# Kernel tuning notes

Measured on AMD Instinct MI355X. Metric: run time of the kernel, lower is better.

The kernel has to match this reference:

```python
import jax, jax.numpy as jnp
import numpy as np

D_MODEL = 1024
N_HEADS = 16
HEAD_DIM = D_MODEL // N_HEADS
ROPE_THETA = 10000.0


def setup_inputs() -> dict:
    key = jax.random.key(0)
    ks = jax.random.split(key, 5)
    B, S = 4, 2048
    x = jax.random.normal(ks[0], (B, S, D_MODEL), dtype=jnp.float32)
    Wq = jax.random.normal(ks[1], (D_MODEL, D_MODEL), dtype=jnp.float32) * 0.02
    Wk = jax.random.normal(ks[2], (D_MODEL, D_MODEL), dtype=jnp.float32) * 0.02
    Wv = jax.random.normal(ks[3], (D_MODEL, D_MODEL), dtype=jnp.float32) * 0.02
    Wo = jax.random.normal(ks[4], (D_MODEL, D_MODEL), dtype=jnp.float32) * 0.02
    token_positions = jnp.arange(S, dtype=jnp.int32)
    return {"x": x, "token_positions": token_positions, "Wq": Wq, "Wk": Wk, "Wv": Wv, "Wo": Wo}


def apply_rope(t, positions):
    # t: [B, H, S, Dk]; positions: [S]
    half = HEAD_DIM // 2
    inv_freq = 1.0 / (ROPE_THETA ** (jnp.arange(half, dtype=jnp.float32) * 2.0 / HEAD_DIM))
    angles = positions.astype(jnp.float32)[:, None] * inv_freq[None, :]  # [S, half]
    cos = jnp.cos(angles)[None, None]  # [1,1,S,half]
    sin = jnp.sin(angles)[None, None]
    t_even = t[..., 0::2]
    t_odd = t[..., 1::2]
    rot_even = t_even * cos - t_odd * sin
    rot_odd = t_even * sin + t_odd * cos
    out = jnp.stack([rot_even, rot_odd], axis=-1)  # [B,H,S,half,2]
    return out.reshape(t.shape)


def reference(x, token_positions, Wq, Wk, Wv, Wo):
    B, S, _ = x.shape
    H, Dk = N_HEADS, HEAD_DIM
    # QKV projections, split heads -> [B, H, S, Dk]
    q = (x @ Wq).reshape(B, S, H, Dk).transpose(0, 2, 1, 3)
    k = (x @ Wk).reshape(B, S, H, Dk).transpose(0, 2, 1, 3)
    v = (x @ Wv).reshape(B, S, H, Dk).transpose(0, 2, 1, 3)
    q = apply_rope(q, token_positions)
    k = apply_rope(k, token_positions)
    scale = 1.0 / jnp.sqrt(jnp.asarray(Dk, dtype=x.dtype))
    scores = jnp.einsum('bhqd,bhkd->bhqk', q, k) * scale
    causal = jnp.tril(jnp.ones((S, S), dtype=bool))
    scores = jnp.where(causal[None, None], scores, jnp.asarray(-jnp.inf, dtype=scores.dtype))
    attn = jax.nn.softmax(scores, axis=-1)
    ctx = jnp.einsum('bhqk,bhkd->bhqd', attn, v)  # [B,H,S,Dk]
    ctx = ctx.transpose(0, 2, 1, 3).reshape(B, S, H * Dk)
    return ctx @ Wo
```

## Files before the change

kernel.cpp:

```cpp
#include <hip/hip_runtime.h>

typedef unsigned short u16;
typedef unsigned int   u32;
typedef __bf16  bf16x8 __attribute__((ext_vector_type(8)));
typedef float   f32x4  __attribute__((ext_vector_type(4)));
typedef float   f32x16 __attribute__((ext_vector_type(16)));
typedef u16     u16x4  __attribute__((ext_vector_type(4)));
typedef u16     u16x8  __attribute__((ext_vector_type(8)));
typedef u32     u32x4  __attribute__((ext_vector_type(4)));

#define D_MODEL 1024
#define N_HEADS 16
#define HEAD_DIM 64
#define BATCH 4
#define SEQ 2048
#define MROWS (BATCH*SEQ)

__device__ __forceinline__ u16 f2bf(float f){
  unsigned u = __builtin_bit_cast(unsigned, f);
  u += 0x7fffu + ((u >> 16) & 1u);
  return (u16)(u >> 16);
}
__device__ __forceinline__ float bf2f(u16 h){
  unsigned u = ((unsigned)h) << 16;
  return __builtin_bit_cast(float, u);
}
__device__ __forceinline__ u32 cvtpk(float a, float b){
  u32 r; asm("v_cvt_pk_bf16_f32 %0, %1, %2" : "=v"(r) : "v"(a), "v"(b)); return r;
}
__device__ __forceinline__ void gload_lds16(const u16* g, u16* l){
  __builtin_amdgcn_global_load_lds((const __attribute__((address_space(1))) void*)g,
                                   (__attribute__((address_space(3))) void*)l, 16, 0, 0);
}

__global__ void k_cvt_x(const float* __restrict__ x, u16* __restrict__ xb, int n4){
  int i = blockIdx.x * 256 + threadIdx.x;
  if (i >= n4) return;
  float4 v = reinterpret_cast<const float4*>(x)[i];
  u16x4 o;
  o.x = f2bf(v.x); o.y = f2bf(v.y); o.z = f2bf(v.z); o.w = f2bf(v.w);
  *reinterpret_cast<u16x4*>(xb + (size_t)i * 4) = o;
}

__global__ void k_transpose_w(const float* __restrict__ Wq, const float* __restrict__ Wk,
                              const float* __restrict__ Wv, const float* __restrict__ Wo,
                              u16* __restrict__ wt){
  __shared__ float t[32][33];
  int z = blockIdx.z;
  const float* W = (z==0)?Wq:(z==1)?Wk:(z==2)?Wv:Wo;
  u16* O = wt + (size_t)z * (D_MODEL*(size_t)D_MODEL);
  int n0 = blockIdx.x*32, k0 = blockIdx.y*32;
  int tx = threadIdx.x, ty = threadIdx.y;
  #pragma unroll
  for (int i = ty; i < 32; i += 8) t[i][tx] = W[(size_t)(k0+i)*D_MODEL + n0 + tx];
  __syncthreads();
  #pragma unroll
  for (int i = ty; i < 32; i += 8){
    int n = n0 + i;
    int np = n;
    if (z < 2){ int d = n & 63; np = (n & ~63) | ((d & 1) << 5) | (d >> 1); }
    O[(size_t)np*D_MODEL + k0 + tx] = f2bf(t[tx][i]);
  }
}

__global__ void k_rope_tab(const int* __restrict__ pos, float2* __restrict__ tab){
  int i = blockIdx.x * 256 + threadIdx.x;
  int s = i >> 5, f = i & 31;
  float inv = exp2f(-(float)f * (13.287712379549449f / 32.0f));
  float a = (float)pos[s] * inv;
  float sn, cs;
  sincosf(a, &sn, &cs);
  tab[i] = make_float2(cs, sn);
}

template<int MODE>
__global__ __launch_bounds__(256, 4) void k_gemm3(const u16* __restrict__ A, const u16* __restrict__ Bt,
                                                  const float2* __restrict__ tab,
                                                  u16* __restrict__ qout, u16* __restrict__ kout,
                                                  u16* __restrict__ vout, float* __restrict__ fout){
  __shared__ u16 sh[3*8192];
  const int K = 1024;
  int tid = threadIdx.x, lane = tid & 63, w = tid >> 6;
  int lr = lane & 15, lg = lane >> 4;
  int m0 = blockIdx.x * 128, n0 = blockIdx.y * 128;
  int wm = w >> 1, wn = w & 1;
  int srow = lane >> 2, scol = (lane & 3) * 8;
  const u16* ga = A  + (size_t)(m0 + w*16 + srow)*K + scol;
  const u16* gb = Bt + (size_t)(n0 + w*16 + srow)*K + scol;
  f32x4 acc[4][4] = {};

#define STG(off, t) { u16* Sb = sh + (off); \
    gload_lds16(ga + (size_t)(t)*32,        Sb + w*512); \
    gload_lds16(ga + (size_t)(t)*32 + 64*K, Sb + 2048 + w*512); \
    gload_lds16(gb + (size_t)(t)*32,        Sb + 4096 + w*512); \
    gload_lds16(gb + (size_t)(t)*32 + 64*K, Sb + 6144 + w*512); }

#define CMP(off) { const u16* Sb = sh + (off); \
    bf16x8 af[4], bv[4]; \
    _Pragma("unroll") \
    for (int mi = 0; mi < 4; mi++) \
      af[mi] = *(const bf16x8*)&Sb[(wm*64 + mi*16 + lr)*32 + lg*8]; \
    _Pragma("unroll") \
    for (int ni = 0; ni < 4; ni++) \
      bv[ni] = *(const bf16x8*)&Sb[4096 + (wn*64 + ni*16 + lr)*32 + lg*8]; \
    _Pragma("unroll") \
    for (int mi = 0; mi < 4; mi++){ \
      _Pragma("unroll") \
      for (int ni = 0; ni < 4; ni++) \
        acc[mi][ni] = __builtin_amdgcn_mfma_f32_16x16x32_bf16(af[mi], bv[ni], acc[mi][ni], 0, 0, 0); \
    } }

  STG(0, 0)
  STG(8192, 1)
  int oc = 0, on = 8192, os = 16384;
  #pragma unroll 1
  for (int t = 0; t < 31; ++t){
    asm volatile("s_waitcnt vmcnt(4) lgkmcnt(0)" ::: "memory");
    __builtin_amdgcn_s_barrier();
    __builtin_amdgcn_sched_barrier(0);
    if (t < 30){ STG(os, t+2) }
    CMP(oc)
    int tmp = oc; oc = on; on = os; os = tmp;
  }
  asm volatile("s_waitcnt vmcnt(0) lgkmcnt(0)" ::: "memory");
  __builtin_amdgcn_s_barrier();
  __builtin_amdgcn_sched_barrier(0);
  CMP(oc)
#undef STG
#undef CMP

  const int which = n0 >> 10;
  #pragma unroll
  for (int mi = 0; mi < 4; mi++){
    int row = m0 + wm*64 + mi*16 + lg*4;
    #pragma unroll
    for (int ni = 0; ni < 4; ni++){
      int col = n0 + wn*64 + ni*16 + lr;
      f32x4 vv = acc[mi][ni];
      if (MODE == 1){
        #pragma unroll
        for (int r = 0; r < 4; r++)
          fout[(size_t)(row + r)*1024 + col] = vv[r];
      } else {
        int cm = col & 1023;
        int hh = cm >> 6, d = cm & 63;
        f32x4 vp = acc[mi][ni ^ 2];
        #pragma unroll
        for (int r = 0; r < 4; r++){
          int rr = row + r;
          int bb = rr >> 11, s = rr & (SEQ-1);
          float val = vv[r];
          if (which < 2){
            float e = (ni < 2) ? val : vp[r];
            float o = (ni < 2) ? vp[r] : val;
            float2 cs = tab[s*32 + ((ni & 1) << 4) + lr];
            float ov = (ni < 2) ? (e*cs.x - o*cs.y) : (e*cs.y + o*cs.x);
            if (which == 0){
              ov *= 0.18033688011112042f;
              qout[(size_t)rr*1024 + cm] = f2bf(ov);
            } else {
              kout[(((size_t)(bb*N_HEADS + hh))*SEQ + s)*64 + d] = f2bf(ov);
            }
          } else {
            vout[(((size_t)(bb*N_HEADS + hh))*(SEQ/16) + (s >> 4))*1024 + d*16 + (s & 15)] = f2bf(val);
          }
        }
      }
    }
  }
}

__global__ __launch_bounds__(256, 3) void k_attn(const u16* __restrict__ q, const u16* __restrict__ k2,
                                                 const u16* __restrict__ v2, u16* __restrict__ ctx){
  __shared__ u16 kv[2][4096];
  const int lane = threadIdx.x & 63, w = threadIdx.x >> 6;
  const int lq = lane & 31, hl = lane >> 5;
  const int B = blockIdx.x;
  const int bh = B & 63, g = 15 - (B >> 6);
  const int b = bh >> 4, h = bh & 15;
  const int qi = 4*g + w;
  const int q0 = qi * 32;
  const int qmax0 = (4*g + 3) * 32;
  const u16* kglob = k2 + (size_t)bh*SEQ*64;
  const u16* vglob = v2 + (size_t)bh*(SEQ/16)*1024;

  const u16* qr_ = q + (size_t)(b*SEQ + q0 + lq)*D_MODEL + h*HEAD_DIM + hl*8;
  bf16x8 qf0 = *(const bf16x8*)&qr_[0];
  bf16x8 qf1 = *(const bf16x8*)&qr_[16];
  bf16x8 qf2 = *(const bf16x8*)&qr_[32];
  bf16x8 qf3 = *(const bf16x8*)&qr_[48];
  f32x16 acc0 = {}, acc1 = {};
  float m = -3.0e38f, l = 0.f;

  auto STAGE = [&](int bf, int jt){
    const u16* ks = kglob + (size_t)(jt + (w<<3) + (lane>>3))*64 + (((lane&7)^(lane>>3))<<3);
    gload_lds16(ks, &kv[bf][w<<9]);
    const u16* vs = vglob + ((size_t)(jt>>4)<<10) + (w<<9) + (lane<<3);
    gload_lds16(vs, &kv[bf][2048 + (w<<9)]);
  };

  STAGE(0, 0);
  __syncthreads();
  int p = 0;
  for (int j0 = 0; j0 <= qmax0; j0 += 32){
    if (j0 + 32 <= qmax0) STAGE(p^1, j0 + 32);
    if (j0 <= q0){
      const char* kb = (const char*)&kv[p][0];
      bf16x8 kf0 = *(const bf16x8*)(kb + lq*128 + (((0+hl) ^ (lq&7))<<4));
      bf16x8 kf1 = *(const bf16x8*)(kb + lq*128 + (((2+hl) ^ (lq&7))<<4));
      bf16x8 kf2 = *(const bf16x8*)(kb + lq*128 + (((4+hl) ^ (lq&7))<<4));
      bf16x8 kf3 = *(const bf16x8*)(kb + lq*128 + (((6+hl) ^ (lq&7))<<4));
      const char* vb = kb + 4096;
      bf16x8 vf00 = *(const bf16x8*)(vb + lq*32 + hl*16);
      bf16x8 vf01 = *(const bf16x8*)(vb + lq*32 + hl*16 + 1024);
      bf16x8 vf10 = *(const bf16x8*)(vb + lq*32 + hl*16 + 2048);
      bf16x8 vf11 = *(const bf16x8*)(vb + lq*32 + hl*16 + 3072);

      f32x16 S = {};
      S = __builtin_amdgcn_mfma_f32_32x32x16_bf16(kf0, qf0, S, 0, 0, 0);
      S = __builtin_amdgcn_mfma_f32_32x32x16_bf16(kf1, qf1, S, 0, 0, 0);
      S = __builtin_amdgcn_mfma_f32_32x32x16_bf16(kf2, qf2, S, 0, 0, 0);
      S = __builtin_amdgcn_mfma_f32_32x32x16_bf16(kf3, qf3, S, 0, 0, 0);

      if (j0 == q0){
        #pragma unroll
        for (int r = 0; r < 16; ++r){
          int kk = (r & 3) + 8*(r >> 2) + 4*hl;
          if (kk > lq) S[r] = -3.0e38f;
        }
      }
      float a0 = fmaxf(fmaxf(S[0],S[1]),  fmaxf(S[2],S[3]));
      float a1 = fmaxf(fmaxf(S[4],S[5]),  fmaxf(S[6],S[7]));
      float a2 = fmaxf(fmaxf(S[8],S[9]),  fmaxf(S[10],S[11]));
      float a3 = fmaxf(fmaxf(S[12],S[13]),fmaxf(S[14],S[15]));
      float pm = fmaxf(fmaxf(a0,a1), fmaxf(a2,a3));
      pm = fmaxf(pm, __shfl_xor(pm, 32));
      if (__any(pm > m + 8.f)){
        float mn = fmaxf(m, pm);
        float cr = __builtin_amdgcn_exp2f(m - mn);
        l *= cr;
        #pragma unroll
        for (int r = 0; r < 16; ++r){ acc0[r] *= cr; acc1[r] *= cr; }
        m = mn;
      }
      #pragma unroll
      for (int r = 0; r < 16; ++r) S[r] = __builtin_amdgcn_exp2f(S[r] - m);
      float s0_ = (S[0]+S[1]) + (S[2]+S[3]);
      float s1_ = (S[4]+S[5]) + (S[6]+S[7]);
      float s2_ = (S[8]+S[9]) + (S[10]+S[11]);
      float s3_ = (S[12]+S[13]) + (S[14]+S[15]);
      l += (s0_+s1_) + (s2_+s3_);
      u32 g0a = cvtpk(S[0], S[1]),  g0b = cvtpk(S[2], S[3]);
      u32 g1a = cvtpk(S[4], S[5]),  g1b = cvtpk(S[6], S[7]);
      u32 g2a = cvtpk(S[8], S[9]),  g2b = cvtpk(S[10],S[11]);
      u32 g3a = cvtpk(S[12],S[13]), g3b = cvtpk(S[14],S[15]);
      u32 s0a = hl ? g0a : g1a, s0b = hl ? g0b : g1b;
      u32 e0a = (u32)__shfl_xor((int)s0a, 32), e0b = (u32)__shfl_xor((int)s0b, 32);
      u32 m0a = hl ? g1a : g0a, m0b = hl ? g1b : g0b;
      u32 s1a = hl ? g2a : g3a, s1b = hl ? g2b : g3b;
      u32 e1a = (u32)__shfl_xor((int)s1a, 32), e1b = (u32)__shfl_xor((int)s1b, 32);
      u32 m1a = hl ? g3a : g2a, m1b = hl ? g3b : g2b;
      u32x4 A0 = { hl ? e0a : m0a, hl ? e0b : m0b, hl ? m0a : e0a, hl ? m0b : e0b };
      u32x4 A1 = { hl ? e1a : m1a, hl ? e1b : m1b, hl ? m1a : e1a, hl ? m1b : e1b };
      bf16x8 pa0 = __builtin_bit_cast(bf16x8, A0);
      bf16x8 pa1 = __builtin_bit_cast(bf16x8, A1);
      acc0 = __builtin_amdgcn_mfma_f32_32x32x16_bf16(vf00, pa0, acc0, 0, 0, 0);
      acc0 = __builtin_amdgcn_mfma_f32_32x32x16_bf16(vf10, pa1, acc0, 0, 0, 0);
      acc1 = __builtin_amdgcn_mfma_f32_32x32x16_bf16(vf01, pa0, acc1, 0, 0, 0);
      acc1 = __builtin_amdgcn_mfma_f32_32x32x16_bf16(vf11, pa1, acc1, 0, 0, 0);
    }
    __syncthreads();
    p ^= 1;
  }
  l += __shfl_xor(l, 32);
  float inv = __builtin_amdgcn_rcpf(l);
  char* tbc = (char*)kv + w*4096;
  #pragma unroll
  for (int r = 0; r < 16; ++r){
    int d0 = (r & 3) + 8*(r >> 2) + 4*hl;
    *(u16*)(tbc + lq*128 + ((2*d0)      ^ ((lq & 7) << 4))) = f2bf(acc0[r] * inv);
    *(u16*)(tbc + lq*128 + ((2*(d0+32)) ^ ((lq & 7) << 4))) = f2bf(acc1[r] * inv);
  }
  int qr2 = lane >> 1, chb = (lane & 1) * 4;
  u16* cp = ctx + (size_t)(b*SEQ + q0 + qr2)*D_MODEL + h*HEAD_DIM;
  #pragma unroll
  for (int i = 0; i < 4; ++i){
    int ch = chb + i;
    u16x8 vv = *(const u16x8*)(tbc + qr2*128 + 16*(ch ^ (qr2 & 7)));
    *(u16x8*)&cp[ch*8] = vv;
  }
}

extern "C" void kernel_launch(void* const* d_in, const int* in_sizes, int n_in,
                              void* d_out, int out_size, void* d_ws, size_t ws_size,
                              hipStream_t stream){
  const float* x  = (const float*)d_in[0];
  const int*  pos = (const int*)d_in[1];
  const float* Wq = (const float*)d_in[2];
  const float* Wk = (const float*)d_in[3];
  const float* Wv = (const float*)d_in[4];
  const float* Wo = (const float*)d_in[5];
  float* out = (float*)d_out;
  char* ws = (char*)d_ws;
  u16* xb   = (u16*)(ws);
  u16* wt   = (u16*)(ws + 16777216);
  u16* qb   = (u16*)(ws + 25165824);
  u16* kbh  = (u16*)(ws + 41943040);
  u16* vt2  = (u16*)(ws + 58720256);
  float2* tab = (float2*)(ws + 75497472);
  u16* ctxb = xb;

  k_cvt_x<<<(MROWS*D_MODEL/4)/256, 256, 0, stream>>>(x, xb, MROWS*D_MODEL/4);
  k_transpose_w<<<dim3(32,32,4), dim3(32,8), 0, stream>>>(Wq, Wk, Wv, Wo, wt);
  k_rope_tab<<<(SEQ*32)/256, 256, 0, stream>>>(pos, tab);
  k_gemm3<0><<<dim3(64,24), 256, 0, stream>>>(xb, wt, tab, qb, kbh, vt2, nullptr);
  k_attn<<<dim3(1024), 256, 0, stream>>>(qb, kbh, vt2, ctxb);
  k_gemm3<1><<<dim3(64,8), 256, 0, stream>>>(ctxb, wt + 3145728, nullptr, nullptr, nullptr, nullptr, out);
}
```

Before: 185.4 us.

## Add dedicated 128x256 QKV GEMM kernel with swizzled LDS and interleaved loads

Replaces the templated QKV projection GEMM with a new 512-thread kernel that computes 128x256 output tiles, so each A tile is reused across twice as many columns. It XOR-swizzles the LDS layout to reduce bank conflicts, interleaves the next-stage global-to-LDS loads between MFMA groups, and raises wave priority around the MFMA blocks. The output GEMM becomes a plain non-templated kernel. The larger tile uses more LDS and registers per block and halves the number of column blocks, which may limit occupancy.

```diff
diff --git a/kernel.cpp b/kernel.cpp
--- a/kernel.cpp
+++ b/kernel.cpp
@@ -32,6 +32,7 @@
   __builtin_amdgcn_global_load_lds((const __attribute__((address_space(1))) void*)g,
                                    (__attribute__((address_space(3))) void*)l, 16, 0, 0);
 }
+#define MFMA16(a,b,c) __builtin_amdgcn_mfma_f32_16x16x32_bf16((a),(b),(c),0,0,0)
 
 __global__ void k_cvt_x(const float* __restrict__ x, u16* __restrict__ xb, int n4){
   int i = blockIdx.x * 256 + threadIdx.x;
@@ -73,11 +74,117 @@
   tab[i] = make_float2(cs, sn);
 }
 
-template<int MODE>
+__global__ __launch_bounds__(512, 4) void k_gqkv(const u16* __restrict__ A, const u16* __restrict__ Bt,
+                                                 const float2* __restrict__ tab,
+                                                 u16* __restrict__ qout, u16* __restrict__ kout,
+                                                 u16* __restrict__ vout){
+  __shared__ u16 sh[3*12288];
+  const int tid = threadIdx.x, lane = tid & 63, w = tid >> 6;
+  const int lr = lane & 15, lg = lane >> 4;
+  const int m0 = blockIdx.x * 128, n0 = blockIdx.y * 256;
+  const int wm = w >> 2, wn = w & 3;
+  const int ra = tid >> 2;
+  const int sca = ((tid & 3) ^ ((ra >> 1) & 3)) << 3;
+  const u16* gA  = A  + (size_t)(m0 + ra)*1024 + sca;
+  const u16* gB0 = Bt + (size_t)(n0 + ra)*1024 + sca;
+  const int rb1 = 128 + ra;
+  const u16* gB1 = Bt + (size_t)(n0 + rb1)*1024 + (((tid & 3) ^ ((rb1 >> 1) & 3)) << 3);
+  const int dA  = w*512;
+  const int dB0 = 4096 + w*512;
+  const int dB1 = 8192 + w*512;
+  int aoff[4], boff[4];
+  #pragma unroll
+  for (int mi = 0; mi < 4; ++mi){ int r_ = wm*64 + mi*16 + lr; aoff[mi] = r_*32 + ((lg ^ ((r_>>1)&3)) << 3); }
+  #pragma unroll
+  for (int ni = 0; ni < 4; ++ni){ int r_ = wn*64 + ni*16 + lr; boff[ni] = 4096 + r_*32 + ((lg ^ ((r_>>1)&3)) << 3); }
+
+  f32x4 acc[4][4] = {};
+#define SA_(base, t)  gload_lds16(gA  + (size_t)(t)*32, sh + (base) + dA)
+#define SB0_(base, t) gload_lds16(gB0 + (size_t)(t)*32, sh + (base) + dB0)
+#define SB1_(base, t) gload_lds16(gB1 + (size_t)(t)*32, sh + (base) + dB1)
+  SA_(0,0); SB0_(0,0); SB1_(0,0);
+  SA_(12288,1); SB0_(12288,1); SB1_(12288,1);
+  int b0 = 0, b1 = 12288, b2 = 24576;
+  #pragma unroll 1
+  for (int t = 0; t < 32; ++t){
+    if (t < 31) { asm volatile("s_waitcnt vmcnt(3) lgkmcnt(0)" ::: "memory"); }
+    else        { asm volatile("s_waitcnt vmcnt(0) lgkmcnt(0)" ::: "memory"); }
+    __builtin_amdgcn_s_barrier();
+    __builtin_amdgcn_sched_barrier(0);
+    const u16* Sb = sh + b0;
+    bf16x8 af0 = *(const bf16x8*)&Sb[aoff[0]];
+    bf16x8 af1 = *(const bf16x8*)&Sb[aoff[1]];
+    bf16x8 af2 = *(const bf16x8*)&Sb[aoff[2]];
+    bf16x8 af3 = *(const bf16x8*)&Sb[aoff[3]];
+    bf16x8 vb0 = *(const bf16x8*)&Sb[boff[0]];
+    bf16x8 vb1 = *(const bf16x8*)&Sb[boff[1]];
+    if (t < 30){ SA_(b2, t+2); }
+    __builtin_amdgcn_s_setprio(1);
+    acc[0][0] = MFMA16(af0, vb0, acc[0][0]);
+    acc[1][0] = MFMA16(af1, vb0, acc[1][0]);
+    acc[2][0] = MFMA16(af2, vb0, acc[2][0]);
+    acc[3][0] = MFMA16(af3, vb0, acc[3][0]);
+    acc[0][1] = MFMA16(af0, vb1, acc[0][1]);
+    acc[1][1] = MFMA16(af1, vb1, acc[1][1]);
+    acc[2][1] = MFMA16(af2, vb1, acc[2][1]);
+    acc[3][1] = MFMA16(af3, vb1, acc[3][1]);
+    __builtin_amdgcn_s_setprio(0);
+    bf16x8 vb2 = *(const bf16x8*)&Sb[boff[2]];
+    bf16x8 vb3 = *(const bf16x8*)&Sb[boff[3]];
+    if (t < 30){ SB0_(b2, t+2); SB1_(b2, t+2); }
+    __builtin_amdgcn_s_setprio(1);
+    acc[0][2] = MFMA16(af0, vb2, acc[0][2]);
+    acc[1][2] = MFMA16(af1, vb2, acc[1][2]);
+    acc[2][2] = MFMA16(af2, vb2, acc[2][2]);
+    acc[3][2] = MFMA16(af3, vb2, acc[3][2]);
+    acc[0][3] = MFMA16(af0, vb3, acc[0][3]);
+    acc[1][3] = MFMA16(af1, vb3, acc[1][3]);
+    acc[2][3] = MFMA16(af2, vb3, acc[2][3]);
+    acc[3][3] = MFMA16(af3, vb3, acc[3][3]);
+    __builtin_amdgcn_s_setprio(0);
+    int tmp = b0; b0 = b1; b1 = b2; b2 = tmp;
+  }
+#undef SA_
+#undef SB0_
+#undef SB1_
+
+  const int which = n0 >> 10;
+  #pragma unroll
+  for (int mi = 0; mi < 4; mi++){
+    int row = m0 + wm*64 + mi*16 + lg*4;
+    #pragma unroll
+    for (int ni = 0; ni < 4; ni++){
+      int col = n0 + wn*64 + ni*16 + lr;
+      int cm = col & 1023;
+      int hh = cm >> 6, d = cm & 63;
+      f32x4 vv = acc[mi][ni];
+      f32x4 vp = acc[mi][ni ^ 2];
+      #pragma unroll
+      for (int r = 0; r < 4; r++){
+        int rr = row + r;
+        int bb = rr >> 11, s = rr & (SEQ-1);
+        float val = vv[r];
+        if (which < 2){
+          float e = (ni < 2) ? val : vp[r];
+          float o = (ni < 2) ? vp[r] : val;
+          float2 cs = tab[s*32 + ((ni & 1) << 4) + lr];
+          float ov = (ni < 2) ? (e*cs.x - o*cs.y) : (e*cs.y + o*cs.x);
+          if (which == 0){
+            ov *= 0.18033688011112042f;
+            qout[(size_t)rr*1024 + cm] = f2bf(ov);
+          } else {
+            kout[(((size_t)(bb*N_HEADS + hh))*SEQ + s)*64 + d] = f2bf(ov);
+          }
+        } else {
+          vout[(((size_t)(bb*N_HEADS + hh))*(SEQ/16) + (s >> 4))*1024 + d*16 + (s & 15)] = f2bf(val);
+        }
+      }
+    }
+  }
+}
+
 __global__ __launch_bounds__(256, 4) void k_gemm3(const u16* __restrict__ A, const u16* __restrict__ Bt,
-                                                  const float2* __restrict__ tab,
-                                                  u16* __restrict__ qout, u16* __restrict__ kout,
-                                                  u16* __restrict__ vout, float* __restrict__ fout){
+                                                  float* __restrict__ fout){
   __shared__ u16 sh[3*8192];
   const int K = 1024;
   int tid = threadIdx.x, lane = tid & 63, w = tid >> 6;
@@ -107,7 +214,7 @@
     for (int mi = 0; mi < 4; mi++){ \
       _Pragma("unroll") \
       for (int ni = 0; ni < 4; ni++) \
-        acc[mi][ni] = __builtin_amdgcn_mfma_f32_16x16x32_bf16(af[mi], bv[ni], acc[mi][ni], 0, 0, 0); \
+        acc[mi][ni] = MFMA16(af[mi], bv[ni], acc[mi][ni]); \
     } }
 
   STG(0, 0)
@@ -129,7 +236,6 @@
 #undef STG
 #undef CMP
 
-  const int which = n0 >> 10;
   #pragma unroll
   for (int mi = 0; mi < 4; mi++){
     int row = m0 + wm*64 + mi*16 + lg*4;
@@ -137,35 +243,9 @@
     for (int ni = 0; ni < 4; ni++){
       int col = n0 + wn*64 + ni*16 + lr;
       f32x4 vv = acc[mi][ni];
-      if (MODE == 1){
-        #pragma unroll
-        for (int r = 0; r < 4; r++)
-          fout[(size_t)(row + r)*1024 + col] = vv[r];
-      } else {
-        int cm = col & 1023;
-        int hh = cm >> 6, d = cm & 63;
-        f32x4 vp = acc[mi][ni ^ 2];
-        #pragma unroll
-        for (int r = 0; r < 4; r++){
-          int rr = row + r;
-          int bb = rr >> 11, s = rr & (SEQ-1);
-          float val = vv[r];
-          if (which < 2){
-            float e = (ni < 2) ? val : vp[r];
-            float o = (ni < 2) ? vp[r] : val;
-            float2 cs = tab[s*32 + ((ni & 1) << 4) + lr];
-            float ov = (ni < 2) ? (e*cs.x - o*cs.y) : (e*cs.y + o*cs.x);
-            if (which == 0){
-              ov *= 0.18033688011112042f;
-              qout[(size_t)rr*1024 + cm] = f2bf(ov);
-            } else {
-              kout[(((size_t)(bb*N_HEADS + hh))*SEQ + s)*64 + d] = f2bf(ov);
-            }
-          } else {
-            vout[(((size_t)(bb*N_HEADS + hh))*(SEQ/16) + (s >> 4))*1024 + d*16 + (s & 15)] = f2bf(val);
-          }
-        }
-      }
+      #pragma unroll
+      for (int r = 0; r < 4; r++)
+        fout[(size_t)(row + r)*1024 + col] = vv[r];
     }
   }
 }
@@ -313,7 +393,7 @@
   k_cvt_x<<<(MROWS*D_MODEL/4)/256, 256, 0, stream>>>(x, xb, MROWS*D_MODEL/4);
   k_transpose_w<<<dim3(32,32,4), dim3(32,8), 0, stream>>>(Wq, Wk, Wv, Wo, wt);
   k_rope_tab<<<(SEQ*32)/256, 256, 0, stream>>>(pos, tab);
-  k_gemm3<0><<<dim3(64,24), 256, 0, stream>>>(xb, wt, tab, qb, kbh, vt2, nullptr);
+  k_gqkv<<<dim3(64,12), 512, 0, stream>>>(xb, wt, tab, qb, kbh, vt2);
   k_attn<<<dim3(1024), 256, 0, stream>>>(qb, kbh, vt2, ctxb);
-  k_gemm3<1><<<dim3(64,8), 256, 0, stream>>>(ctxb, wt + 3145728, nullptr, nullptr, nullptr, nullptr, out);
-}
+  k_gemm3<<<dim3(64,8), 256, 0, stream>>>(ctxb, wt + 3145728, out);
+}
```

Measured after the change: 180.7 us. 2.5% less time.
